# Optimization experiments

Measured on AMD Instinct MI355X. Metric: run time of the kernel, lower is better.

The kernel has to match this reference:

```python
import jax, jax.numpy as jnp
import numpy as np

B, I, T = 8192, 128, 21
H1, H2, H3 = 256, 256, 128


def _init(key, shape, fan_in):
    # torch-style uniform(-1/sqrt(fan_in), 1/sqrt(fan_in))
    bound = 1.0 / np.sqrt(fan_in)
    return jax.random.uniform(key, shape, jnp.float32, -bound, bound)


def setup_inputs() -> dict:
    key = jax.random.key(0)
    ks = jax.random.split(key, 16)
    x = jax.random.normal(ks[0], (B, I, T), jnp.float32)
    d = {"x": x}
    # stacked LSTM weights (PyTorch layout: W_ih (4H, in), gate order i,f,g,o)
    d["W1_ih"] = _init(ks[1], (4 * H1, I), H1)
    d["b1_ih"] = _init(ks[2], (4 * H1,), H1)
    d["b1_hh"] = _init(ks[3], (4 * H1,), H1)
    d["W2_ih"] = _init(ks[4], (4 * H2, H1), H2)
    d["b2_ih"] = _init(ks[5], (4 * H2,), H2)
    d["b2_hh"] = _init(ks[6], (4 * H2,), H2)
    d["W3_ih"] = _init(ks[7], (4 * H3, H2), H3)
    d["b3_ih"] = _init(ks[8], (4 * H3,), H3)
    d["b3_hh"] = _init(ks[9], (4 * H3,), H3)
    d["fc1_w"] = _init(ks[10], (1, H3), H3)
    d["fc1_b"] = _init(ks[11], (1,), H3)
    d["fc2_w"] = _init(ks[12], (T, T), T)
    d["fc2_b"] = _init(ks[13], (T,), T)
    return d


def _lstm_cell_step(xt, W_ih, b_ih, b_hh):
    # single timestep with h0 = c0 = 0, so the W_hh @ h0 term vanishes
    gates = xt @ W_ih.T + (b_ih + b_hh)          # (B, 21, 4H)
    i, f, g, o = jnp.split(gates, 4, axis=-1)    # torch gate order i,f,g,o
    c = jax.nn.sigmoid(i) * jnp.tanh(g)          # f * c0 = 0
    return jax.nn.sigmoid(o) * jnp.tanh(c)


def reference(x, W1_ih, b1_ih, b1_hh, W2_ih, b2_ih, b2_hh,
              W3_ih, b3_ih, b3_hh, fc1_w, fc1_b, fc2_w, fc2_b):
    # fold the 21 independent single-step columns into the batch dim
    xt = jnp.transpose(x, (0, 2, 1))             # (B, 21, I)
    h1 = _lstm_cell_step(xt, W1_ih, b1_ih, b1_hh)   # (B, 21, H1)
    h2 = _lstm_cell_step(h1, W2_ih, b2_ih, b2_hh)   # (B, 21, H2)
    h3 = _lstm_cell_step(h2, W3_ih, b3_ih, b3_hh)   # (B, 21, H3)
    y = h3 @ fc1_w.T + fc1_b                     # (B, 21, 1)
    y = y[..., 0][:, None, :]                    # (B, 1, 21)  == x_torch
    out = y @ fc2_w.T + fc2_b                    # (B, 1, 21)
    return out
```

## Files before the change

kernel.cpp:

```cpp
#include <hip/hip_runtime.h>
#include <hip/hip_bf16.h>
#include <stdint.h>


typedef __attribute__((ext_vector_type(8))) short bf16x8;
typedef __attribute__((ext_vector_type(4))) float f32x4;

#define M_ROWS 172032
#define BATCH  8192

__device__ __forceinline__ float bf2f(unsigned short u) {
    union { unsigned int i; float f; } v; v.i = ((unsigned int)u) << 16; return v.f;
}
__device__ __forceinline__ unsigned short f2bf(float f) {
    union { float f; unsigned int i; } v; v.f = f;
    unsigned int r = v.i + 0x7fffu + ((v.i >> 16) & 1u);
    return (unsigned short)(r >> 16);
}
__device__ __forceinline__ float sigmoidf_(float x) {
    return __builtin_amdgcn_rcpf(1.0f + __expf(-x));
}
__device__ __forceinline__ float tanhf_(float x) {
    x = fminf(fmaxf(x, -20.0f), 20.0f);
    float e = __expf(-2.0f * x);
    return (1.0f - e) * __builtin_amdgcn_rcpf(1.0f + e);
}

__device__ __forceinline__ void gload_lds16(const unsigned short* g, unsigned short* l) {
    __builtin_amdgcn_global_load_lds(
        (const __attribute__((address_space(1))) unsigned int*)g,
        (__attribute__((address_space(3))) unsigned int*)l,
        16, 0, 0);
}

__global__ __launch_bounds__(256) void k_convert(
    const float* __restrict__ src, unsigned short* __restrict__ dst, int n4)
{
    int i = blockIdx.x * 256 + threadIdx.x;
    if (i < n4) {
        float4 v = ((const float4*)src)[i];
        ushort4 o;
        o.x = f2bf(v.x); o.y = f2bf(v.y); o.z = f2bf(v.z); o.w = f2bf(v.w);
        ((ushort4*)dst)[i] = o;
    }
}

__global__ __launch_bounds__(256) void k_transpose(
    const float* __restrict__ x, unsigned short* __restrict__ xt)
{
    __shared__ unsigned short tile[128 * 22];
    const int b = blockIdx.x, tid = threadIdx.x;
    const float* xb = x + (size_t)b * 2688;
    for (int idx = tid; idx < 2688; idx += 256) {
        int i = idx / 21, t = idx - i * 21;
        tile[i * 22 + t] = f2bf(xb[idx]);
    }
    __syncthreads();
    unsigned short* xtb = xt + (size_t)b * 2688;
    for (int idx = tid; idx < 2688; idx += 256) {
        int t = idx >> 7, i = idx & 127;
        xtb[t * 128 + i] = tile[i * 22 + t];
    }
}

template<int K, int HG>
__global__ __launch_bounds__(256, 3) void k_gemm_act(
    const unsigned short* __restrict__ A,
    const unsigned short* __restrict__ W,
    const float* __restrict__ bih,
    const float* __restrict__ bhh,
    unsigned short* __restrict__ Hout)
{
    __shared__ __align__(16) unsigned short As[128 * 64];
    __shared__ __align__(16) unsigned short Ws[192 * 64];
    __shared__ float Bs[192];

    const int tid  = threadIdx.x;
    const int wave = tid >> 6;
    const int lane = tid & 63;
    const int wm = wave >> 1;
    const int wn = wave & 1;
    const int c0 = blockIdx.x * 64;
    const int r0 = blockIdx.y * 128;

    const unsigned short* aptr[4];
#pragma unroll
    for (int i = 0; i < 4; ++i) {
        int q16 = (wave * 4 + i) * 64 + lane;
        int row = q16 >> 3, pslot = q16 & 7;
        int lslot = pslot ^ (row & 7);
        aptr[i] = A + (size_t)(r0 + row) * K + lslot * 8;
    }
    const unsigned short* wptr[6];
#pragma unroll
    for (int i = 0; i < 6; ++i) {
        int q16 = (wave * 6 + i) * 64 + lane;
        int lrow = q16 >> 3, pslot = q16 & 7;
        int lslot = pslot ^ (lrow & 7);
        int gate = lrow >> 6, n = lrow & 63;
        int gbase = (gate == 0) ? 0 : (gate + 1) * HG;
        wptr[i] = W + (size_t)(gbase + c0 + n) * K + lslot * 8;
    }

    if (tid < 192) {
        int g = tid >> 6, c = tid & 63;
        int gbase = (g == 0) ? 0 : (g + 1) * HG;
        int idx = gbase + c0 + c;
        Bs[tid] = bih[idx] + bhh[idx];
    }

    f32x4 acc[3][4][2];
#pragma unroll
    for (int g = 0; g < 3; ++g)
#pragma unroll
        for (int m = 0; m < 4; ++m)
#pragma unroll
            for (int n = 0; n < 2; ++n)
                acc[g][m][n] = (f32x4){0.f, 0.f, 0.f, 0.f};

#pragma unroll
    for (int kk = 0; kk < K; kk += 64) {
        if (kk) __syncthreads();
#pragma unroll
        for (int i = 0; i < 4; ++i)
            gload_lds16(aptr[i] + kk, &As[(wave * 4 + i) * 512]);
#pragma unroll
        for (int i = 0; i < 6; ++i)
            gload_lds16(wptr[i] + kk, &Ws[(wave * 6 + i) * 512]);
        __syncthreads();

#pragma unroll
        for (int ks = 0; ks < 64; ks += 32) {
            bf16x8 af[4];
            bf16x8 bfr[3][2];
            const int rsel = lane & 15;
            const int slot = (ks >> 3) | (lane >> 4);
            const int soff = (slot ^ (rsel & 7)) * 8;
#pragma unroll
            for (int m = 0; m < 4; ++m)
                af[m] = *(const bf16x8*)&As[(wm * 64 + m * 16 + rsel) * 64 + soff];
#pragma unroll
            for (int g = 0; g < 3; ++g)
#pragma unroll
                for (int n = 0; n < 2; ++n)
                    bfr[g][n] = *(const bf16x8*)&Ws[(g * 64 + wn * 32 + n * 16 + rsel) * 64 + soff];
#pragma unroll
            for (int g = 0; g < 3; ++g)
#pragma unroll
                for (int m = 0; m < 4; ++m)
#pragma unroll
                    for (int n = 0; n < 2; ++n)
                        acc[g][m][n] = __builtin_amdgcn_mfma_f32_16x16x32_bf16(
                            af[m], bfr[g][n], acc[g][m][n], 0, 0, 0);
        }
    }

    const int quad = lane >> 4;
    const int csel = lane & 15;
#pragma unroll
    for (int m = 0; m < 4; ++m) {
#pragma unroll
        for (int n = 0; n < 2; ++n) {
            int cloc = wn * 32 + n * 16 + csel;
            float bi = Bs[cloc], bg = Bs[64 + cloc], bo = Bs[128 + cloc];
            f32x4 vi = acc[0][m][n], vg = acc[1][m][n], vo = acc[2][m][n];
#pragma unroll
            for (int r = 0; r < 4; ++r) {
                int row = r0 + wm * 64 + m * 16 + quad * 4 + r;
                float cv = sigmoidf_(vi[r] + bi) * tanhf_(vg[r] + bg);
                float h  = sigmoidf_(vo[r] + bo) * tanhf_(cv);
                Hout[(size_t)row * HG + c0 + cloc] = f2bf(h);
            }
        }
    }
}

#define FSTR 169
__global__ __launch_bounds__(256) void k_final(
    const unsigned short* __restrict__ h3,
    const float* __restrict__ fc1w,
    const float* __restrict__ fc1b,
    const float* __restrict__ fc2w,
    const float* __restrict__ fc2b,
    float* __restrict__ out)
{
    __shared__ unsigned short ht[128 * FSTR];
    __shared__ float fwl[128];
    __shared__ float yl[168];
    __shared__ float f2l[441];
    __shared__ float f2bl[21];

    const int tid = threadIdx.x;
    const int b0 = blockIdx.x * 8;

    if (tid < 128) fwl[tid] = fc1w[tid];
    for (int i = tid; i < 441; i += 256) f2l[i] = fc2w[i];
    if (tid < 21) f2bl[tid] = fc2b[tid];

    const unsigned int* hsrc = (const unsigned int*)(h3 + (size_t)b0 * 2688);
    for (int gi = tid; gi < 10752; gi += 256) {
        unsigned int v = hsrc[gi];
        int e = gi * 2;
        int task = e >> 7;
        int c = e & 127;
        ht[c * FSTR + task] = (unsigned short)(v & 0xffffu);
        ht[(c + 1) * FSTR + task] = (unsigned short)(v >> 16);
    }
    __syncthreads();

    const float f1b = fc1b[0];
    if (tid < 168) {
        float s = f1b;
#pragma unroll 8
        for (int c = 0; c < 128; ++c)
            s += fwl[c] * bf2f(ht[c * FSTR + tid]);
        yl[tid] = s;
    }
    __syncthreads();
    if (tid < 168) {
        int bloc = tid / 21;
        int tp = tid - bloc * 21;
        float s = f2bl[tp];
#pragma unroll
        for (int t = 0; t < 21; ++t)
            s += yl[bloc * 21 + t] * f2l[tp * 21 + t];
        out[(size_t)(b0 + bloc) * 21 + tp] = s;
    }
}

extern "C" void kernel_launch(void* const* d_in, const int* in_sizes, int n_in,
                              void* d_out, int out_size, void* d_ws, size_t ws_size,
                              hipStream_t stream)
{
    const float* x    = (const float*)d_in[0];
    const float* W1   = (const float*)d_in[1];
    const float* b1i  = (const float*)d_in[2];
    const float* b1h  = (const float*)d_in[3];
    const float* W2   = (const float*)d_in[4];
    const float* b2i  = (const float*)d_in[5];
    const float* b2h  = (const float*)d_in[6];
    const float* W3   = (const float*)d_in[7];
    const float* b3i  = (const float*)d_in[8];
    const float* b3h  = (const float*)d_in[9];
    const float* fc1w = (const float*)d_in[10];
    const float* fc1b = (const float*)d_in[11];
    const float* fc2w = (const float*)d_in[12];
    const float* fc2b = (const float*)d_in[13];
    float* out = (float*)d_out;

    unsigned short* Wc1 = (unsigned short*)d_ws;
    unsigned short* Wc2 = Wc1 + 131072;
    unsigned short* Wc3 = Wc2 + 262144;
    unsigned short* buf = Wc3 + 131072;

    int C = 1;
    while (C < 64 && 1048576 + (size_t)(M_ROWS / C) * 1536 > ws_size) C <<= 1;
    const int R  = M_ROWS / C;
    const int Bc = BATCH / C;

    unsigned short* xt = buf;
    unsigned short* h1 = xt + (size_t)R * 128;
    unsigned short* h2 = h1 + (size_t)R * 256;
    unsigned short* h3 = h2 + (size_t)R * 256;

    k_convert<<<128, 256, 0, stream>>>(W1, Wc1, 32768);
    k_convert<<<256, 256, 0, stream>>>(W2, Wc2, 65536);
    k_convert<<<128, 256, 0, stream>>>(W3, Wc3, 32768);

    for (int c = 0; c < C; ++c) {
        const float* xc = x + (size_t)c * Bc * 2688;
        k_transpose<<<Bc, 256, 0, stream>>>(xc, xt);
        k_gemm_act<128, 256><<<dim3(4, R / 128), 256, 0, stream>>>(xt, Wc1, b1i, b1h, h1);
        k_gemm_act<256, 256><<<dim3(4, R / 128), 256, 0, stream>>>(h1, Wc2, b2i, b2h, h2);
        k_gemm_act<256, 128><<<dim3(2, R / 128), 256, 0, stream>>>(h2, Wc3, b3i, b3h, h3);
        k_final<<<Bc / 8, 256, 0, stream>>>(h3, fc1w, fc1b, fc2w, fc2b,
                                            out + (size_t)c * Bc * 21);
    }
}
```

Measured before the change: 435.6 us.

## Fuse LSTM activations with Padé tanh, register biases, swap grid order

Replaces separate sigmoid/tanh calls with a fused LSTM output function that uses exp2 intrinsics, a shared reciprocal and a rational Padé approximation for tanh of the cell state. Biases are read directly into registers instead of staged through shared memory. Occupancy hint is raised from 3 to 4 and the grid is transposed so row tiles vary fastest. The grid swap may hurt L2 reuse of the activation rows, and the Padé tanh slightly changes numerics.

```diff
diff --git a/kernel.cpp b/kernel.cpp
--- a/kernel.cpp
+++ b/kernel.cpp
@@ -17,13 +17,20 @@
     unsigned int r = v.i + 0x7fffu + ((v.i >> 16) & 1u);
     return (unsigned short)(r >> 16);
 }
-__device__ __forceinline__ float sigmoidf_(float x) {
-    return __builtin_amdgcn_rcpf(1.0f + __expf(-x));
-}
-__device__ __forceinline__ float tanhf_(float x) {
-    x = fminf(fmaxf(x, -20.0f), 20.0f);
-    float e = __expf(-2.0f * x);
-    return (1.0f - e) * __builtin_amdgcn_rcpf(1.0f + e);
+
+#define LOG2E  1.44269504f
+#define LOG2E2 2.88539008f
+
+__device__ __forceinline__ float lstm_h(float gi, float gg, float go) {
+    gg = fminf(fmaxf(gg, -15.0f), 15.0f);
+    float Eg = __builtin_amdgcn_exp2f(gg * LOG2E2);
+    float Ei = __builtin_amdgcn_exp2f(-gi * LOG2E);
+    float c  = (Eg - 1.0f) * __builtin_amdgcn_rcpf((Eg + 1.0f) * (1.0f + Ei));
+    float Eo = __builtin_amdgcn_exp2f(-go * LOG2E);
+    float c2 = c * c;
+    float num = c * fmaf(c2, c2 + 105.0f, 945.0f);
+    float den = fmaf(c2, fmaf(15.0f, c2, 420.0f), 945.0f);
+    return num * __builtin_amdgcn_rcpf(den * (1.0f + Eo));
 }
 
 __device__ __forceinline__ void gload_lds16(const unsigned short* g, unsigned short* l) {
@@ -64,7 +71,7 @@
 }
 
 template<int K, int HG>
-__global__ __launch_bounds__(256, 3) void k_gemm_act(
+__global__ __launch_bounds__(256, 4) void k_gemm_act(
     const unsigned short* __restrict__ A,
     const unsigned short* __restrict__ W,
     const float* __restrict__ bih,
@@ -73,15 +80,15 @@
 {
     __shared__ __align__(16) unsigned short As[128 * 64];
     __shared__ __align__(16) unsigned short Ws[192 * 64];
-    __shared__ float Bs[192];
 
     const int tid  = threadIdx.x;
     const int wave = tid >> 6;
     const int lane = tid & 63;
     const int wm = wave >> 1;
     const int wn = wave & 1;
-    const int c0 = blockIdx.x * 64;
-    const int r0 = blockIdx.y * 128;
+    const int r0 = blockIdx.x * 128;
+    const int c0 = blockIdx.y * 64;
+    const int csel = lane & 15;
 
     const unsigned short* aptr[4];
 #pragma unroll
@@ -102,11 +109,13 @@
         wptr[i] = W + (size_t)(gbase + c0 + n) * K + lslot * 8;
     }
 
-    if (tid < 192) {
-        int g = tid >> 6, c = tid & 63;
-        int gbase = (g == 0) ? 0 : (g + 1) * HG;
-        int idx = gbase + c0 + c;
-        Bs[tid] = bih[idx] + bhh[idx];
+    float bias[3][2];
+#pragma unroll
+    for (int n = 0; n < 2; ++n) {
+        int cloc = c0 + wn * 32 + n * 16 + csel;
+        bias[0][n] = bih[cloc] + bhh[cloc];
+        bias[1][n] = bih[2 * HG + cloc] + bhh[2 * HG + cloc];
+        bias[2][n] = bih[3 * HG + cloc] + bhh[3 * HG + cloc];
     }
 
     f32x4 acc[3][4][2];
@@ -156,19 +165,17 @@
     }
 
     const int quad = lane >> 4;
-    const int csel = lane & 15;
 #pragma unroll
     for (int m = 0; m < 4; ++m) {
 #pragma unroll
         for (int n = 0; n < 2; ++n) {
             int cloc = wn * 32 + n * 16 + csel;
-            float bi = Bs[cloc], bg = Bs[64 + cloc], bo = Bs[128 + cloc];
             f32x4 vi = acc[0][m][n], vg = acc[1][m][n], vo = acc[2][m][n];
 #pragma unroll
             for (int r = 0; r < 4; ++r) {
                 int row = r0 + wm * 64 + m * 16 + quad * 4 + r;
-                float cv = sigmoidf_(vi[r] + bi) * tanhf_(vg[r] + bg);
-                float h  = sigmoidf_(vo[r] + bo) * tanhf_(cv);
+                float h = lstm_h(vi[r] + bias[0][n], vg[r] + bias[1][n],
+                                 vo[r] + bias[2][n]);
                 Hout[(size_t)row * HG + c0 + cloc] = f2bf(h);
             }
         }
@@ -270,9 +277,9 @@
     for (int c = 0; c < C; ++c) {
         const float* xc = x + (size_t)c * Bc * 2688;
         k_transpose<<<Bc, 256, 0, stream>>>(xc, xt);
-        k_gemm_act<128, 256><<<dim3(4, R / 128), 256, 0, stream>>>(xt, Wc1, b1i, b1h, h1);
-        k_gemm_act<256, 256><<<dim3(4, R / 128), 256, 0, stream>>>(h1, Wc2, b2i, b2h, h2);
-        k_gemm_act<256, 128><<<dim3(2, R / 128), 256, 0, stream>>>(h2, Wc3, b3i, b3h, h3);
+        k_gemm_act<128, 256><<<dim3(R / 128, 4), 256, 0, stream>>>(xt, Wc1, b1i, b1h, h1);
+        k_gemm_act<256, 256><<<dim3(R / 128, 4), 256, 0, stream>>>(h1, Wc2, b2i, b2h, h2);
+        k_gemm_act<256, 128><<<dim3(R / 128, 2), 256, 0, stream>>>(h2, Wc3, b3i, b3h, h3);
         k_final<<<Bc / 8, 256, 0, stream>>>(h3, fc1w, fc1b, fc2w, fc2b,
                                             out + (size_t)c * Bc * 21);
     }
```

Measured after the change: 768.8 us. 76.5% more time.
